# Performance work log

Hardware: AMD Instinct MI355X
Metric: run time of the kernel (lower is better)

Reference implementation:

```python
import jax, jax.numpy as jnp
import numpy as np

MAX_DEPTH = 6
NUM_TREES = 64
LEAF_DIMS = 128
D_IN = 512
BATCH = 4096
N_INTERNAL = 2 ** MAX_DEPTH - 1  # 63
N_LEAVES = 2 ** MAX_DEPTH        # 64


def setup_inputs() -> dict:
    key = jax.random.key(0)
    ks = jax.random.split(key, 4)
    x = jax.random.normal(ks[0], (BATCH, D_IN), dtype=jnp.float32)
    # Stacked internal-node dense layers, node i at index i (level order, node_index ordering)
    W = jax.random.normal(ks[1], (N_INTERNAL, D_IN, NUM_TREES), dtype=jnp.float32) / np.sqrt(D_IN)
    b = jnp.zeros((N_INTERNAL, NUM_TREES), dtype=jnp.float32)
    leaf_weight = jax.random.normal(ks[2], (N_LEAVES, LEAF_DIMS, NUM_TREES), dtype=jnp.float32)
    gates = jax.random.normal(ks[3], (N_LEAVES, LEAF_DIMS, NUM_TREES), dtype=jnp.float32)
    return {"x": x, "W": W, "b": b, "leaf_weight": leaf_weight, "gates": gates}


def reference(x, W, b, leaf_weight, gates):
    # All internal-node gating probabilities in one batched matmul:
    # g[b, n, t] = sigmoid(x[b] @ W[n] + b[n])  for every internal node n, tree t
    g = jax.nn.sigmoid(jnp.einsum('bd,ndt->bnt', x, W) + b[None, :, :])  # [B, 63, T]

    B = x.shape[0]
    T = W.shape[-1]
    # Path probability to each leaf, built level by level.
    # Level l has 2^l nodes at internal indices [2^l - 1, 2^(l+1) - 2];
    # interleaving (left=p*g, right=p*(1-g)) matches node_index child ordering.
    p = jnp.ones((B, 1, T), dtype=x.dtype)
    for level in range(MAX_DEPTH):
        start = 2 ** level - 1
        n_lvl = 2 ** level
        gl = g[:, start:start + n_lvl, :]                  # [B, n_lvl, T]
        children = jnp.stack([p * gl, p * (1.0 - gl)], axis=2)  # [B, n_lvl, 2, T]
        p = children.reshape(B, 2 * n_lvl, T)
    # p: [B, n_leaves, T] leaf path probabilities

    # Softmax mixture-of-experts gate over trees, then weighted leaf mixture:
    # out[b, d] = sum_{l, t} p[b, l, t] * leaf_weight[l, d, t] * softmax(gates, -1)[l, d, t]
    w = leaf_weight * jax.nn.softmax(gates, axis=-1)  # [L, D, T]
    out = jnp.einsum('blt,ldt->bd', p, w)
    return out
```

## Files before the change

kernel.cpp:

```cpp
#include <hip/hip_runtime.h>
#include <stdint.h>

#define BATCH 4096
#define DIN   512
#define NT    64
#define NL    64
#define LD    128

typedef __attribute__((ext_vector_type(8))) short bf16x8;
typedef __attribute__((ext_vector_type(8))) _Float16 f16x8;
typedef __attribute__((ext_vector_type(4))) float f32x4;

typedef const __attribute__((address_space(1))) unsigned char* gcp_t;
typedef __attribute__((address_space(3))) unsigned char* lp_t;

__device__ __forceinline__ void gl_lds16(const void* g, void* l) {
  __builtin_amdgcn_global_load_lds((gcp_t)g, (lp_t)l, 16, 0, 0);
}

__device__ __forceinline__ unsigned pk_bf16(float a, float b) {
  union { float f; unsigned u; } ua, ub;
  ua.f = a; ub.f = b;
  return __builtin_amdgcn_perm(ub.u + 0x8000u, ua.u + 0x8000u, 0x07060302u);
}

__global__ __launch_bounds__(256) void prep_all_k(
    const float* __restrict__ x, const float* __restrict__ W,
    const float* __restrict__ gates, const float* __restrict__ lw,
    unsigned short* __restrict__ xb, unsigned short* __restrict__ Wt,
    unsigned short* __restrict__ Wv2, float* __restrict__ out) {
  __shared__ float smem[12288];
  const int bx = blockIdx.x;
  const int tid = threadIdx.x;

  if (bx < 2048) {
    int i = bx * 256 + tid;
    float4 v = ((const float4*)x)[i];
    uint2 o;
    o.x = pk_bf16(v.x, v.y);
    o.y = pk_bf16(v.z, v.w);
    ((uint2*)xb)[i] = o;
  } else if (bx < 2304) {
    int bb = bx - 2048;
    int n = bb >> 2, d0 = (bb & 3) * 128;
    float* buf = smem;
    if (n < 63) {
      for (int it = 0; it < 32; ++it) {
        int idx = it * 256 + tid;
        buf[idx] = W[n * 32768 + (d0 + (idx >> 6)) * 64 + (idx & 63)];
      }
    }
    __syncthreads();
    int t = tid >> 2, q = tid & 3;
    unsigned vals[16];
    #pragma unroll
    for (int j = 0; j < 16; ++j) {
      float va = (n < 63) ? buf[(q * 32 + 2 * j) * 64 + t] : 0.0f;
      float vb = (n < 63) ? buf[(q * 32 + 2 * j + 1) * 64 + t] : 0.0f;
      vals[j] = (n < 63) ? pk_bf16(va, vb) : 0u;
    }
    uint4* dst = (uint4*)(Wt + t * 32768 + n * 512 + d0 + q * 32);
    const uint4* src = (const uint4*)vals;
    dst[0] = src[0]; dst[1] = src[1]; dst[2] = src[2]; dst[3] = src[3];
  } else if (bx < 2432) {
    int d = bx - 2304;
    float* gb = smem;
    float* lb = smem + 4096;
    float* wv = smem + 8192;
    for (int it = 0; it < 16; ++it) {
      int idx = it * 256 + tid;
      int l = idx >> 6;
      int ga = l * 8192 + d * 64 + (idx & 63);
      gb[idx] = gates[ga];
      lb[idx] = lw[ga];
    }
    __syncthreads();
    int wave = tid >> 6, lane = tid & 63;
    for (int l = wave; l < 64; l += 4) {
      float v = gb[l * 64 + lane];
      float mx = v;
      for (int m = 32; m >= 1; m >>= 1) mx = fmaxf(mx, __shfl_xor(mx, m));
      float e = __expf(v - mx);
      float s = e;
      for (int m = 32; m >= 1; m >>= 1) s += __shfl_xor(s, m);
      wv[l * 64 + lane] = lb[l * 64 + lane] * e / s;
    }
    __syncthreads();
    #pragma unroll
    for (int c = 0; c < 2; ++c) {
      int k0 = tid * 16 + c * 8;
      unsigned o[4];
      #pragma unroll
      for (int j = 0; j < 4; ++j) {
        int ka = k0 + 2 * j, kb = k0 + 2 * j + 1;
        o[j] = pk_bf16(wv[(ka & 63) * 64 + (ka >> 6)], wv[(kb & 63) * 64 + (kb >> 6)]);
      }
      *(uint4*)(Wv2 + (long)d * 4096 + k0) = *(const uint4*)o;
    }
  } else {
    float4 z = {0.f, 0.f, 0.f, 0.f};
    int base = (bx - 2432) * 256 + tid;
    float4* o4 = (float4*)out;
    #pragma unroll
    for (int k = 0; k < 16; ++k)
      o4[k * 8192 + base] = z;
  }
}

__global__ __launch_bounds__(256, 4) void gemm1_tree_k(
    const unsigned short* __restrict__ xb,
    const unsigned short* __restrict__ Wt,
    const float* __restrict__ bias,
    unsigned short* __restrict__ P)
{
  __shared__ __align__(16) char smem[32768];
  unsigned short* AsB = (unsigned short*)smem;
  unsigned short* BsB = (unsigned short*)(smem + 16384);
  _Float16* gbuf = (_Float16*)smem;

  const int tid = threadIdx.x;
  const int wave = tid >> 6, lane = tid & 63;

  const int lin = blockIdx.x + (blockIdx.y << 5);
  const int rr = lin & 7, kk_ = lin >> 3;
  const int b0 = (((kk_ & 7) | ((rr & 3) << 3))) * 128;
  const int t0 = (((kk_ >> 3) | ((rr >> 2) << 4))) * 2;

  const int wm = (wave >> 1) * 64, wn = (wave & 1) * 64;
  const int mrow = lane & 15, kg = lane >> 4;
  const int slot = (kg ^ ((mrow >> 1) & 3)) * 8;

  float bv[4];
  #pragma unroll
  for (int j = 0; j < 4; ++j) {
    int n = j * 16 + mrow;
    bv[j] = (n < 63) ? bias[n * 64 + t0 + (wave & 1)] : 0.0f;
  }

  const f32x4 zero = {0.f, 0.f, 0.f, 0.f};
  f32x4 acc[4][4];
  #pragma unroll
  for (int i = 0; i < 4; ++i)
    #pragma unroll
    for (int j = 0; j < 4; ++j) acc[i][j] = zero;

  const int g0 = wave * 64 + lane;
  const int g1 = g0 + 256;
  const int c0 = ((g0 & 3) ^ ((g0 >> 3) & 3)) * 8;
  const int c1 = ((g1 & 3) ^ ((g1 >> 3) & 3)) * 8;
  const unsigned short* Ag0 = xb + (long)(b0 + (g0 >> 2)) * 512 + c0;
  const unsigned short* Ag1 = xb + (long)(b0 + (g1 >> 2)) * 512 + c1;
  const unsigned short* Bg0 = Wt + (long)(t0 * 64 + (g0 >> 2)) * 512 + c0;
  const unsigned short* Bg1 = Wt + (long)(t0 * 64 + (g1 >> 2)) * 512 + c1;
  const int lofs0 = wave * 512;
  const int lofs1 = wave * 512 + 2048;

  gl_lds16(Ag0, AsB + lofs0);
  gl_lds16(Ag1, AsB + lofs1);
  gl_lds16(Bg0, BsB + lofs0);
  gl_lds16(Bg1, BsB + lofs1);

  for (int it = 0; it < 16; ++it) {
    const int buf = (it & 1) * 4096;
    if (it < 15) {
      const int kk = (it + 1) * 32;
      const int nbuf = ((it + 1) & 1) * 4096;
      gl_lds16(Ag0 + kk, AsB + nbuf + lofs0);
      gl_lds16(Ag1 + kk, AsB + nbuf + lofs1);
      gl_lds16(Bg0 + kk, BsB + nbuf + lofs0);
      gl_lds16(Bg1 + kk, BsB + nbuf + lofs1);
      asm volatile("s_waitcnt vmcnt(4)" ::: "memory");
    } else {
      asm volatile("s_waitcnt vmcnt(0)" ::: "memory");
    }
    asm volatile("s_barrier" ::: "memory");

    bf16x8 fa[4], fb[4];
    #pragma unroll
    for (int i = 0; i < 4; ++i)
      fa[i] = *(const bf16x8*)(AsB + buf + (wm + i * 16 + mrow) * 32 + slot);
    #pragma unroll
    for (int j = 0; j < 4; ++j)
      fb[j] = *(const bf16x8*)(BsB + buf + (wn + j * 16 + mrow) * 32 + slot);
    #pragma unroll
    for (int i = 0; i < 4; ++i)
      #pragma unroll
      for (int j = 0; j < 4; ++j)
        acc[i][j] = __builtin_amdgcn_mfma_f32_16x16x32_bf16(fa[i], fb[j], acc[i][j], 0, 0, 0);

    asm volatile("s_waitcnt lgkmcnt(0)" ::: "memory");
    asm volatile("s_barrier" ::: "memory");
  }

  #pragma unroll
  for (int i = 0; i < 4; ++i)
    #pragma unroll
    for (int j = 0; j < 4; ++j) {
      int col = wn + j * 16 + mrow;
      int oct = col >> 3, sub = col & 7;
      #pragma unroll
      for (int r = 0; r < 4; ++r) {
        int row = wm + i * 16 + kg * 4 + r;
        float z = acc[i][j][r] + bv[j];
        gbuf[row * 128 + ((oct ^ (row & 15)) << 3) + sub] =
            (_Float16)__builtin_amdgcn_rcpf(1.0f + __expf(-z));
      }
    }
  __syncthreads();

  {
    const int row = tid >> 1, tr = tid & 1;
    const _Float16* grow = gbuf + row * 128;
    const int rx = row & 15;
    float g[63];
    #pragma unroll
    for (int c = 0; c < 8; ++c) {
      f16x8 gv = *(const f16x8*)(grow + (((tr * 8 + c) ^ rx) << 3));
      #pragma unroll
      for (int j = 0; j < 8; ++j) {
        int n = c * 8 + j;
        if (n < 63) g[n] = (float)gv[j];
      }
    }
    float P3[8];
    {
      float a0 = g[0],            a1 = 1.0f - g[0];
      float c0_ = a0 * g[1],      c1_ = a0 * (1.0f - g[1]);
      float c2_ = a1 * g[2],      c3_ = a1 * (1.0f - g[2]);
      P3[0] = c0_ * g[3];  P3[1] = c0_ * (1.0f - g[3]);
      P3[2] = c1_ * g[4];  P3[3] = c1_ * (1.0f - g[4]);
      P3[4] = c2_ * g[5];  P3[5] = c2_ * (1.0f - g[5]);
      P3[6] = c3_ * g[6];  P3[7] = c3_ * (1.0f - g[6]);
    }
    unsigned short* prow = P + (long)(b0 + row) * 4096 + (t0 + tr) * 64;
    #pragma unroll
    for (int o = 0; o < 8; ++o) {
      float g3 = g[7 + o];
      float q0 = P3[o] * g3, q1 = P3[o] * (1.0f - g3);
      float g4a = g[15 + 2 * o], g4b = g[16 + 2 * o];
      float r0 = q0 * g4a, r1 = q0 * (1.0f - g4a);
      float r2 = q1 * g4b, r3 = q1 * (1.0f - g4b);
      unsigned ou[4];
      #pragma unroll
      for (int h = 0; h < 4; ++h) {
        float g5 = g[31 + 4 * o + h];
        float rr2 = (h == 0) ? r0 : (h == 1) ? r1 : (h == 2) ? r2 : r3;
        ou[h] = pk_bf16(rr2 * g5, rr2 * (1.0f - g5));
      }
      *(uint4*)(prow + o * 8) = *(const uint4*)ou;
    }
  }
}

__global__ __launch_bounds__(256, 4) void gemm2_k(
    const unsigned short* __restrict__ P,
    const unsigned short* __restrict__ Wv2,
    float* __restrict__ out)
{
  __shared__ unsigned short AsB[2][64 * 32];
  __shared__ unsigned short BsB[2][128 * 32];
  const int tid = threadIdx.x;
  const int wave = tid >> 6, lane = tid & 63;
  const int b0 = blockIdx.x * 64;
  const int k0 = blockIdx.y * 1024;

  const f32x4 zero = {0.f, 0.f, 0.f, 0.f};
  f32x4 acc[2][4];
  #pragma unroll
  for (int i = 0; i < 2; ++i)
    #pragma unroll
    for (int j = 0; j < 4; ++j) acc[i][j] = zero;

  const int g0 = wave * 64 + lane;
  const int g1 = g0 + 256;
  const int c0 = ((g0 & 3) ^ ((g0 >> 3) & 3)) * 8;
  const int c1 = ((g1 & 3) ^ ((g1 >> 3) & 3)) * 8;
  const unsigned short* Ag0 = P + (long)(b0 + (g0 >> 2)) * 4096 + k0 + c0;
  const unsigned short* Bg0 = Wv2 + (long)(g0 >> 2) * 4096 + k0 + c0;
  const unsigned short* Bg1 = Wv2 + (long)(g1 >> 2) * 4096 + k0 + c1;
  const int lofs = wave * 512;

  const int wm = (wave >> 1) * 32, wn = (wave & 1) * 64;
  const int mrow = lane & 15, kg = lane >> 4;
  const int slot = (kg ^ ((mrow >> 1) & 3)) * 8;

  gl_lds16(Ag0, AsB[0] + lofs);
  gl_lds16(Bg0, BsB[0] + lofs);
  gl_lds16(Bg1, BsB[0] + lofs + 2048);

  for (int it = 0; it < 32; ++it) {
    const int buf = it & 1;
    if (it < 31) {
      const int kk = (it + 1) * 32;
      const int nbuf = (it + 1) & 1;
      gl_lds16(Ag0 + kk, AsB[nbuf] + lofs);
      gl_lds16(Bg0 + kk, BsB[nbuf] + lofs);
      gl_lds16(Bg1 + kk, BsB[nbuf] + lofs + 2048);
      asm volatile("s_waitcnt vmcnt(3)" ::: "memory");
    } else {
      asm volatile("s_waitcnt vmcnt(0)" ::: "memory");
    }
    asm volatile("s_barrier" ::: "memory");

    bf16x8 fa[2], fb[4];
    #pragma unroll
    for (int i = 0; i < 2; ++i)
      fa[i] = *(const bf16x8*)(AsB[buf] + (wm + i * 16 + mrow) * 32 + slot);
    #pragma unroll
    for (int j = 0; j < 4; ++j)
      fb[j] = *(const bf16x8*)(BsB[buf] + (wn + j * 16 + mrow) * 32 + slot);
    #pragma unroll
    for (int i = 0; i < 2; ++i)
      #pragma unroll
      for (int j = 0; j < 4; ++j)
        acc[i][j] = __builtin_amdgcn_mfma_f32_16x16x32_bf16(fa[i], fb[j], acc[i][j], 0, 0, 0);

    asm volatile("s_waitcnt lgkmcnt(0)" ::: "memory");
    asm volatile("s_barrier" ::: "memory");
  }

  #pragma unroll
  for (int i = 0; i < 2; ++i)
    #pragma unroll
    for (int j = 0; j < 4; ++j) {
      int col = wn + j * 16 + mrow;
      #pragma unroll
      for (int r = 0; r < 4; ++r) {
        int row = wm + i * 16 + kg * 4 + r;
        atomicAdd(&out[(long)(b0 + row) * 128 + col], acc[i][j][r]);
      }
    }
}

extern "C" void kernel_launch(void* const* d_in, const int* in_sizes, int n_in,
                              void* d_out, int out_size, void* d_ws, size_t ws_size,
                              hipStream_t stream) {
  const float* x     = (const float*)d_in[0];
  const float* W     = (const float*)d_in[1];
  const float* b     = (const float*)d_in[2];
  const float* lw    = (const float*)d_in[3];
  const float* gates = (const float*)d_in[4];
  float* out = (float*)d_out;

  char* ws = (char*)d_ws;
  unsigned short* xb  = (unsigned short*)(ws);
  unsigned short* Wt  = (unsigned short*)(ws + (4l  << 20));
  unsigned short* Wv2 = (unsigned short*)(ws + (8l  << 20));
  unsigned short* P   = (unsigned short*)(ws + (16l << 20));

  hipLaunchKernelGGL(prep_all_k,   dim3(2464),   dim3(256), 0, stream,
                     x, W, gates, lw, xb, Wt, Wv2, out);
  hipLaunchKernelGGL(gemm1_tree_k, dim3(32, 32), dim3(256), 0, stream, xb, Wt, b, P);
  hipLaunchKernelGGL(gemm2_k,      dim3(64, 4),  dim3(256), 0, stream, P, Wv2, out);
}
```

Before: 137.0 us.

## Enlarge gemm1 block to 256 batch rows with 512 threads sharing the W tile

The first GEMM plus tree kernel now uses 512-thread blocks that each cover 256 batch rows instead of 128, so the grid shrinks from 1024 to 512 blocks. Each K step still stages one W tile for the block's two trees, but it is now shared by eight waves instead of four, which halves redundant W traffic. The block-to-tile mapping is rewritten and the LDS double buffers are resized; total LDS rises to 64KB per block. The cost is fewer resident blocks per CU, less latency hiding, and a coarser grid with possible tail imbalance. The hidden epilogue must also handle 256 rows correctly.

```diff
diff --git a/kernel.cpp b/kernel.cpp
--- a/kernel.cpp
+++ b/kernel.cpp
@@ -107,24 +107,24 @@
   }
 }
 
-__global__ __launch_bounds__(256, 4) void gemm1_tree_k(
+__global__ __launch_bounds__(512, 4) void gemm1_tree_k(
     const unsigned short* __restrict__ xb,
     const unsigned short* __restrict__ Wt,
     const float* __restrict__ bias,
     unsigned short* __restrict__ P)
 {
-  __shared__ __align__(16) char smem[32768];
+  __shared__ __align__(16) char smem[65536];
   unsigned short* AsB = (unsigned short*)smem;
-  unsigned short* BsB = (unsigned short*)(smem + 16384);
+  unsigned short* BsB = (unsigned short*)(smem + 32768);
   _Float16* gbuf = (_Float16*)smem;
 
   const int tid = threadIdx.x;
   const int wave = tid >> 6, lane = tid & 63;
 
-  const int lin = blockIdx.x + (blockIdx.y << 5);
-  const int rr = lin & 7, kk_ = lin >> 3;
-  const int b0 = (((kk_ & 7) | ((rr & 3) << 3))) * 128;
-  const int t0 = (((kk_ >> 3) | ((rr >> 2) << 4))) * 2;
+  const int lin = blockIdx.x;
+  const int rr = lin & 7, kq = lin >> 3;
+  const int b0 = ((kq & 3) | ((rr & 3) << 2)) * 256;
+  const int t0 = ((kq >> 2) | ((rr >> 2) << 4)) * 2;
 
   const int wm = (wave >> 1) * 64, wn = (wave & 1) * 64;
   const int mrow = lane & 15, kg = lane >> 4;
@@ -144,32 +144,32 @@
     #pragma unroll
     for (int j = 0; j < 4; ++j) acc[i][j] = zero;
 
-  const int g0 = wave * 64 + lane;
-  const int g1 = g0 + 256;
+  const int g0 = tid;
+  const int g1 = tid + 512;
   const int c0 = ((g0 & 3) ^ ((g0 >> 3) & 3)) * 8;
   const int c1 = ((g1 & 3) ^ ((g1 >> 3) & 3)) * 8;
   const unsigned short* Ag0 = xb + (long)(b0 + (g0 >> 2)) * 512 + c0;
   const unsigned short* Ag1 = xb + (long)(b0 + (g1 >> 2)) * 512 + c1;
   const unsigned short* Bg0 = Wt + (long)(t0 * 64 + (g0 >> 2)) * 512 + c0;
-  const unsigned short* Bg1 = Wt + (long)(t0 * 64 + (g1 >> 2)) * 512 + c1;
-  const int lofs0 = wave * 512;
-  const int lofs1 = wave * 512 + 2048;
-
-  gl_lds16(Ag0, AsB + lofs0);
-  gl_lds16(Ag1, AsB + lofs1);
-  gl_lds16(Bg0, BsB + lofs0);
-  gl_lds16(Bg1, BsB + lofs1);
+  const int lofsA0 = wave * 512;
+  const int lofsA1 = wave * 512 + 4096;
+  const int lofsB  = wave * 512;
+
+  gl_lds16(Ag0, AsB + lofsA0);
+  gl_lds16(Ag1, AsB + lofsA1);
+  gl_lds16(Bg0, BsB + lofsB);
 
   for (int it = 0; it < 16; ++it) {
-    const int buf = (it & 1) * 4096;
+    const int bufA = (it & 1) * 8192;
+    const int bufB = (it & 1) * 4096;
     if (it < 15) {
       const int kk = (it + 1) * 32;
-      const int nbuf = ((it + 1) & 1) * 4096;
-      gl_lds16(Ag0 + kk, AsB + nbuf + lofs0);
-      gl_lds16(Ag1 + kk, AsB + nbuf + lofs1);
-      gl_lds16(Bg0 + kk, BsB + nbuf + lofs0);
-      gl_lds16(Bg1 + kk, BsB + nbuf + lofs1);
-      asm volatile("s_waitcnt vmcnt(4)" ::: "memory");
+      const int nA = ((it + 1) & 1) * 8192;
+      const int nB = ((it + 1) & 1) * 4096;
+      gl_lds16(Ag0 + kk, AsB + nA + lofsA0);
+      gl_lds16(Ag1 + kk, AsB + nA + lofsA1);
+      gl_lds16(Bg0 + kk, BsB + nB + lofsB);
+      asm volatile("s_waitcnt vmcnt(3)" ::: "memory");
     } else {
       asm volatile("s_waitcnt vmcnt(0)" ::: "memory");
     }
@@ -178,10 +178,10 @@
     bf16x8 fa[4], fb[4];
     #pragma unroll
     for (int i = 0; i < 4; ++i)
-      fa[i] = *(const bf16x8*)(AsB + buf + (wm + i * 16 + mrow) * 32 + slot);
+      fa[i] = *(const bf16x8*)(AsB + bufA + (wm + i * 16 + mrow) * 32 + slot);
     #pragma unroll
     for (int j = 0; j < 4; ++j)
-      fb[j] = *(const bf16x8*)(BsB + buf + (wn + j * 16 + mrow) * 32 + slot);
+      fb[j] = *(const bf16x8*)(BsB + bufB + (wn + j * 16 + mrow) * 32 + slot);
     #pragma unroll
     for (int i = 0; i < 4; ++i)
       #pragma unroll
@@ -348,8 +348,8 @@
   unsigned short* Wv2 = (unsigned short*)(ws + (8l  << 20));
   unsigned short* P   = (unsigned short*)(ws + (16l << 20));
 
-  hipLaunchKernelGGL(prep_all_k,   dim3(2464),   dim3(256), 0, stream,
+  hipLaunchKernelGGL(prep_all_k,   dim3(2464), dim3(256), 0, stream,
                      x, W, gates, lw, xb, Wt, Wv2, out);
-  hipLaunchKernelGGL(gemm1_tree_k, dim3(32, 32), dim3(256), 0, stream, xb, Wt, b, P);
-  hipLaunchKernelGGL(gemm2_k,      dim3(64, 4),  dim3(256), 0, stream, P, Wv2, out);
-}
+  hipLaunchKernelGGL(gemm1_tree_k, dim3(512),  dim3(512), 0, stream, xb, Wt, b, P);
+  hipLaunchKernelGGL(gemm2_k,      dim3(64, 4), dim3(256), 0, stream, P, Wv2, out);
+}
```

Measured after the change: 136.8 us. No clear change (-0.1%).
